# Kernel tuning notes

Hardware: AMD Instinct MI355X
Metric: run time of the kernel (lower is better)

The kernel has to match this reference:

```python
import jax, jax.numpy as jnp
import numpy as np

B, N, QD = 2, 4096, 512
HEADS, DIM_HEAD = 8, 64
INNER = HEADS * DIM_HEAD  # 512
SCALE = DIM_HEAD ** -0.5


def setup_inputs() -> dict:
    key = jax.random.key(0)
    ks = jax.random.split(key, 6)
    s = 0.02
    return {
        "x": jax.random.normal(ks[0], (B, N, QD), dtype=jnp.float32),
        "Wq": jax.random.normal(ks[1], (QD, INNER), dtype=jnp.float32) * s,
        "Wk": jax.random.normal(ks[2], (QD, INNER), dtype=jnp.float32) * s,
        "Wv": jax.random.normal(ks[3], (QD, INNER), dtype=jnp.float32) * s,
        "Wo": jax.random.normal(ks[4], (INNER, QD), dtype=jnp.float32) * s,
        "bo": jnp.zeros((QD,), dtype=jnp.float32),
    }


def reference(x, Wq, Wk, Wv, Wo, bo):
    # self-attention: context = x; mask = None; attention_sf = False
    q = x @ Wq  # [B, N, INNER]
    k = x @ Wk
    v = x @ Wv
    # split heads: [B, H, N, D]
    def split(t):
        return t.reshape(B, N, HEADS, DIM_HEAD).transpose(0, 2, 1, 3)
    q, k, v = split(q), split(k), split(v)
    # fp32 QK^T (ATTN_PRECISION='fp32' path)
    sim = jnp.einsum('bhid,bhjd->bhij', q.astype(jnp.float32), k.astype(jnp.float32)) * SCALE
    attn = jax.nn.softmax(sim, axis=-1)
    out = jnp.einsum('bhij,bhjd->bhid', attn, v)  # [B, H, N, D]
    out = out.transpose(0, 2, 1, 3).reshape(B, N, INNER)
    return out @ Wo + bo  # Dropout(p=0) is identity
```

## Files before the change

kernel.cpp:

```cpp
#include <hip/hip_runtime.h>
#include <hip/hip_bf16.h>


typedef __attribute__((ext_vector_type(8))) short short8;
typedef __attribute__((ext_vector_type(4))) float floatx4;

#define MFMA16(a, b, c) __builtin_amdgcn_mfma_f32_16x16x32_bf16((a), (b), (c), 0, 0, 0)

#if __has_builtin(__builtin_amdgcn_exp2f)
#define EXP2(x) __builtin_amdgcn_exp2f(x)
#else
#define EXP2(x) exp2f(x)
#endif

#define QSCALE 0.18033688011112042f

static __device__ __forceinline__ unsigned short f2b(float f) {
  unsigned int u = __float_as_uint(f);
  u += 0x7FFFu + ((u >> 16) & 1u);
  return (unsigned short)(u >> 16);
}

static __device__ __forceinline__ unsigned int pkb(float a, float b) {
  float2 t{a, b};
  __hip_bfloat162 h = __float22bfloat162_rn(t);
  union { __hip_bfloat162 h2; unsigned int u; } cv;
  cv.h2 = h;
  return cv.u;
}

static __device__ __forceinline__ void dma16(const unsigned short* g,
                                             unsigned short* l) {
  __builtin_amdgcn_global_load_lds(
      (const __attribute__((address_space(1))) unsigned int*)g,
      (__attribute__((address_space(3))) unsigned int*)l, 16, 0, 0);
}

__global__ __launch_bounds__(256) void prep_kernel(
    const float* __restrict__ Wq, const float* __restrict__ Wk,
    const float* __restrict__ Wv, const float* __restrict__ Wo,
    const float* __restrict__ x, unsigned short* __restrict__ wtq,
    unsigned short* __restrict__ wtk, unsigned short* __restrict__ wtv,
    unsigned short* __restrict__ wto, unsigned short* __restrict__ xb) {
  const int z = blockIdx.z;
  const int tid = threadIdx.x;
  if (z >= 4) {
    const int bid = (z - 4) * 256 + blockIdx.y * 16 + blockIdx.x;
    const int idx = (bid * 256 + tid) * 8;
    const float4 a = *(const float4*)(x + idx);
    const float4 b = *(const float4*)(x + idx + 4);
    unsigned int u[4] = {pkb(a.x, a.y), pkb(a.z, a.w), pkb(b.x, b.y),
                         pkb(b.z, b.w)};
    *(short8*)(xb + idx) = *(short8*)u;
    return;
  }
  const float* __restrict__ W = (z == 0) ? Wq : (z == 1) ? Wk : (z == 2) ? Wv : Wo;
  unsigned short* __restrict__ T = (z == 0) ? wtq : (z == 1) ? wtk : (z == 2) ? wtv : wto;
  const int k0 = blockIdx.x * 32, c0 = blockIdx.y * 32;
  __shared__ float Ts[32][33];
  const int r = tid >> 3, cc = (tid & 7) * 4;
  const float4 v = *(const float4*)(W + (k0 + r) * 512 + c0 + cc);
  Ts[r][cc] = v.x; Ts[r][cc + 1] = v.y; Ts[r][cc + 2] = v.z; Ts[r][cc + 3] = v.w;
  __syncthreads();
  const unsigned long long uu =
      (unsigned long long)pkb(Ts[cc][r], Ts[cc + 1][r]) |
      ((unsigned long long)pkb(Ts[cc + 2][r], Ts[cc + 3][r]) << 32);
  *(unsigned long long*)(T + (c0 + r) * 512 + k0 + cc) = uu;
}

__global__ __launch_bounds__(256) void qkv_fused_kernel(
    const float* __restrict__ x, const unsigned short* __restrict__ wtq,
    const unsigned short* __restrict__ wtk,
    const unsigned short* __restrict__ wtv, unsigned short* __restrict__ qo,
    unsigned short* __restrict__ ko, unsigned short* __restrict__ vo) {
  const int m0 = blockIdx.x * 128;
  const int c0 = blockIdx.y * 64;
  __shared__ __align__(16) unsigned short As[128 * 40];
  __shared__ __align__(16) unsigned short Bs[3][64 * 32];
  const int tid = threadIdx.x;
  const int lane = tid & 63, w = tid >> 6;
  const int i = lane & 15, q = lane >> 4;
  const int wy = w >> 1, wx = w & 1;
  const int arow = tid >> 1, ch = (tid & 1) * 16;
  const int br = w * 16 + (lane >> 2), bc8 = (lane & 3) * 8;
  const unsigned short* bg0 = wtq + (c0 + br) * 512 + bc8;
  const unsigned short* bg1 = wtk + (c0 + br) * 512 + bc8;
  const unsigned short* bg2 = wtv + (c0 + br) * 512 + bc8;
  unsigned short* bd0 = &Bs[0][(w * 16) * 32];
  unsigned short* bd1 = &Bs[1][(w * 16) * 32];
  unsigned short* bd2 = &Bs[2][(w * 16) * 32];
  floatx4 acc[3][4][2] = {};
  for (int k0 = 0; k0 < 512; k0 += 32) {
    dma16(bg0 + k0, bd0);
    dma16(bg1 + k0, bd1);
    dma16(bg2 + k0, bd2);
    {
      const float* src = x + (m0 + arow) * 512 + k0 + ch;
      unsigned int av[8];
#pragma unroll
      for (int j = 0; j < 8; ++j) av[j] = pkb(src[2 * j], src[2 * j + 1]);
      *(short8*)&As[arow * 40 + ch] = *(short8*)&av[0];
      *(short8*)&As[arow * 40 + ch + 8] = *(short8*)&av[4];
    }
    __syncthreads();
    short8 af[4];
#pragma unroll
    for (int t = 0; t < 4; ++t)
      af[t] = *(const short8*)&As[(wy * 64 + t * 16 + i) * 40 + q * 8];
#pragma unroll
    for (int z = 0; z < 3; ++z)
#pragma unroll
      for (int g = 0; g < 2; ++g) {
        const short8 bf =
            *(const short8*)&Bs[z][(wx * 32 + g * 16 + i) * 32 + q * 8];
#pragma unroll
        for (int t = 0; t < 4; ++t)
          acc[z][t][g] = MFMA16(af[t], bf, acc[z][t][g]);
      }
    __syncthreads();
  }
#pragma unroll
  for (int z = 0; z < 3; ++z)
#pragma unroll
    for (int t = 0; t < 4; ++t)
#pragma unroll
      for (int g = 0; g < 2; ++g) {
        const int col = c0 + wx * 32 + g * 16 + i;
        const int h = col >> 6, d = col & 63;
        const int row0 = m0 + wy * 64 + t * 16 + q * 4;
        const int b = row0 >> 12;
        const int n0 = row0 & 4095;
        if (z == 2) {
          unsigned int* dst =
              (unsigned int*)&vo[(((b * 8 + h) * 64 + d) << 12) + n0];
          dst[0] = pkb(acc[z][t][g][0], acc[z][t][g][1]);
          dst[1] = pkb(acc[z][t][g][2], acc[z][t][g][3]);
        } else {
          unsigned short* dst = (z == 0) ? qo : ko;
          const float sc = (z == 0) ? QSCALE : 1.0f;
#pragma unroll
          for (int r = 0; r < 4; ++r)
            dst[(((b * 8 + h) << 12) + (n0 + r)) * 64 + d] =
                f2b(acc[z][t][g][r] * sc);
        }
      }
}

__global__ __launch_bounds__(512, 4) void flash_kernel(
    const unsigned short* __restrict__ Q, const unsigned short* __restrict__ K,
    const unsigned short* __restrict__ Vt, unsigned short* __restrict__ O) {
  const int bh = blockIdx.x;
  const int m0 = blockIdx.y * 128;
  const int tid = threadIdx.x;
  const int lane = tid & 63, w = tid >> 6;
  const int i = lane & 15, q = lane >> 4;
  const int rt = w & 3;
  const int kg = w >> 2;
  const unsigned short* qp = Q + bh * (4096 * 64);
  const unsigned short* kp = K + bh * (4096 * 64);
  const unsigned short* vp = Vt + bh * (64 * 4096);

  __shared__ __align__(16) unsigned short SM[32768];
  unsigned short* Ks = SM + kg * 4096;
  unsigned short* Vs = SM + 8192 + kg * 4096;
  unsigned short* pw = SM + 16384 + w * 2048;

  const int srow = (tid & 255) >> 3;
  const int c0s = tid & 7;
  const int sw8 = (c0s ^ (srow & 7)) * 8;
  const unsigned short* kgp = kp + (kg * 2048 + srow) * 64 + c0s * 8;
  const unsigned short* vgp = vp + srow * 4096 + kg * 2048 + c0s * 8;

  short8 qf[2][2];
#pragma unroll
  for (int t = 0; t < 2; ++t)
#pragma unroll
    for (int kc = 0; kc < 2; ++kc)
      qf[t][kc] = *(const short8*)(qp + (m0 + rt * 32 + t * 16 + i) * 64 +
                                   kc * 32 + q * 8);

  floatx4 accO[2][4] = {};
  floatx4 accL[2] = {};
  short8 ones;
  {
    const short ov = (i == 0) ? (short)0x3F80 : (short)0;
#pragma unroll
    for (int j = 0; j < 8; ++j) ones[j] = ov;
  }
  const floatx4 zf = {0.f, 0.f, 0.f, 0.f};
  const int sl = i & 7;

  *(short8*)&Ks[srow * 64 + sw8] = *(const short8*)(kgp);
  *(short8*)&Ks[(srow + 32) * 64 + sw8] = *(const short8*)(kgp + 32 * 64);
  *(short8*)&Vs[srow * 64 + sw8] = *(const short8*)(vgp);
  *(short8*)&Vs[(srow + 32) * 64 + sw8] = *(const short8*)(vgp + 32 * 4096);
  __syncthreads();

  for (int jt = 0; jt < 32; ++jt) {
    short8 kn0, kn1, vn0, vn1;
    if (jt < 31) {
      kn0 = *(const short8*)(kgp + (jt + 1) * 4096);
      kn1 = *(const short8*)(kgp + (jt + 1) * 4096 + 32 * 64);
      vn0 = *(const short8*)(vgp + (jt + 1) * 64);
      vn1 = *(const short8*)(vgp + (jt + 1) * 64 + 32 * 4096);
    }
#pragma unroll
    for (int g = 0; g < 4; ++g) {
      const short8 kf0 = *(const short8*)(&Ks[(g * 16 + i) * 64 + (q ^ sl) * 8]);
      const short8 kf1 =
          *(const short8*)(&Ks[(g * 16 + i) * 64 + ((4 + q) ^ sl) * 8]);
#pragma unroll
      for (int t = 0; t < 2; ++t) {
        floatx4 s = MFMA16(kf0, qf[t][0], zf);
        s = MFMA16(kf1, qf[t][1], s);
        const float e0 = EXP2(s[0]), e1 = EXP2(s[1]);
        const float e2 = EXP2(s[2]), e3 = EXP2(s[3]);
        *(unsigned long long*)&pw[(t * 16 + i) * 64 +
                                  (((2 * g + (q >> 1)) ^ sl) * 8) +
                                  (q & 1) * 4] =
            (unsigned long long)pkb(e0, e1) |
            ((unsigned long long)pkb(e2, e3) << 32);
      }
    }
    short8 pf[2][2];
#pragma unroll
    for (int t = 0; t < 2; ++t) {
      pf[t][0] = *(const short8*)(pw + (t * 16 + i) * 64 + (q ^ sl) * 8);
      pf[t][1] = *(const short8*)(pw + (t * 16 + i) * 64 + ((4 + q) ^ sl) * 8);
      accL[t] = MFMA16(pf[t][0], ones, accL[t]);
      accL[t] = MFMA16(pf[t][1], ones, accL[t]);
    }
#pragma unroll
    for (int dg = 0; dg < 4; ++dg) {
      const short8 vf0 =
          *(const short8*)(&Vs[(dg * 16 + i) * 64 + (q ^ sl) * 8]);
      const short8 vf1 =
          *(const short8*)(&Vs[(dg * 16 + i) * 64 + ((4 + q) ^ sl) * 8]);
#pragma unroll
      for (int t = 0; t < 2; ++t) {
        accO[t][dg] = MFMA16(pf[t][0], vf0, accO[t][dg]);
        accO[t][dg] = MFMA16(pf[t][1], vf1, accO[t][dg]);
      }
    }
    __syncthreads();
    if (jt < 31) {
      *(short8*)&Ks[srow * 64 + sw8] = kn0;
      *(short8*)&Ks[(srow + 32) * 64 + sw8] = kn1;
      *(short8*)&Vs[srow * 64 + sw8] = vn0;
      *(short8*)&Vs[(srow + 32) * 64 + sw8] = vn1;
    }
    __syncthreads();
  }

  float* MB = (float*)SM;
  if (kg == 1) {
    float* dst = MB + (rt * 64 + lane) * 40;
#pragma unroll
    for (int t = 0; t < 2; ++t) {
#pragma unroll
      for (int dg = 0; dg < 4; ++dg)
#pragma unroll
        for (int r = 0; r < 4; ++r) dst[t * 16 + dg * 4 + r] = accO[t][dg][r];
#pragma unroll
      for (int r = 0; r < 4; ++r) dst[32 + t * 4 + r] = accL[t][r];
    }
  }
  __syncthreads();
  if (kg == 1) return;
  {
    const float* src = MB + (rt * 64 + lane) * 40;
#pragma unroll
    for (int t = 0; t < 2; ++t) {
#pragma unroll
      for (int dg = 0; dg < 4; ++dg)
#pragma unroll
        for (int r = 0; r < 4; ++r) accO[t][dg][r] += src[t * 16 + dg * 4 + r];
#pragma unroll
      for (int r = 0; r < 4; ++r) accL[t][r] += src[32 + t * 4 + r];
    }
  }

  const int b = bh >> 3, h = bh & 7;
#pragma unroll
  for (int t = 0; t < 2; ++t) {
    float inv[4];
#pragma unroll
    for (int r = 0; r < 4; ++r) {
      const float l = __shfl(accL[t][r], lane & 48, 64);
      inv[r] = 1.0f / l;
    }
#pragma unroll
    for (int dg = 0; dg < 4; ++dg)
#pragma unroll
      for (int r = 0; r < 4; ++r) {
        const int n = m0 + rt * 32 + t * 16 + q * 4 + r;
        const int col = h * 64 + dg * 16 + i;
        O[((b << 12) + n) * 512 + col] = f2b(accO[t][dg][r] * inv[r]);
      }
  }
}

__global__ __launch_bounds__(256) void out_proj_kernel(
    const unsigned short* __restrict__ A, const unsigned short* __restrict__ wto,
    const float* __restrict__ bo, float* __restrict__ out) {
  const int m0 = blockIdx.x * 64, c0 = blockIdx.y * 64;
  __shared__ __align__(16) unsigned short As[64 * 32];
  __shared__ __align__(16) unsigned short Bs[64 * 32];
  const int tid = threadIdx.x;
  const int lane = tid & 63, w = tid >> 6;
  const int i = lane & 15, q = lane >> 4;
  const int wy = w >> 1, wx = w & 1;
  const int sr = lane >> 2, sc8 = (lane & 3) * 8;
  const unsigned short* ag = A + (m0 + w * 16 + sr) * 512 + sc8;
  const unsigned short* bg = wto + (c0 + w * 16 + sr) * 512 + sc8;
  unsigned short* adst = &As[(w * 16) * 32];
  unsigned short* bdst = &Bs[(w * 16) * 32];
  floatx4 acc[2][2] = {};
  for (int k0 = 0; k0 < 512; k0 += 32) {
    dma16(ag + k0, adst);
    dma16(bg + k0, bdst);
    __syncthreads();
    short8 af[2], bfr[2];
#pragma unroll
    for (int t = 0; t < 2; ++t)
      af[t] = *(const short8*)&As[(wy * 32 + t * 16 + i) * 32 + q * 8];
#pragma unroll
    for (int g = 0; g < 2; ++g)
      bfr[g] = *(const short8*)&Bs[(wx * 32 + g * 16 + i) * 32 + q * 8];
#pragma unroll
    for (int t = 0; t < 2; ++t)
#pragma unroll
      for (int g = 0; g < 2; ++g) acc[t][g] = MFMA16(af[t], bfr[g], acc[t][g]);
    __syncthreads();
  }
#pragma unroll
  for (int t = 0; t < 2; ++t)
#pragma unroll
    for (int g = 0; g < 2; ++g) {
      const int col = c0 + wx * 32 + g * 16 + i;
      const float bias = bo[col];
#pragma unroll
      for (int r = 0; r < 4; ++r) {
        const int row = m0 + wy * 32 + t * 16 + q * 4 + r;
        out[row * 512 + col] = acc[t][g][r] + bias;
      }
    }
}

extern "C" void kernel_launch(void* const* d_in, const int* in_sizes, int n_in,
                              void* d_out, int out_size, void* d_ws,
                              size_t ws_size, hipStream_t stream) {
  const float* x = (const float*)d_in[0];
  const float* Wq = (const float*)d_in[1];
  const float* Wk = (const float*)d_in[2];
  const float* Wv = (const float*)d_in[3];
  const float* Wo = (const float*)d_in[4];
  const float* bo = (const float*)d_in[5];
  float* out = (float*)d_out;

  const size_t tsz = (size_t)16 * 4096 * 64;
  unsigned short* qws = (unsigned short*)d_ws;
  unsigned short* kws = qws + tsz;
  unsigned short* vws = kws + tsz;
  unsigned short* ows = vws + tsz;
  unsigned short* wtq = ows + tsz;
  unsigned short* wtk = wtq + 512 * 512;
  unsigned short* wtv = wtk + 512 * 512;
  unsigned short* wto = wtv + 512 * 512;
  unsigned short* xb = wto + 512 * 512;

  prep_kernel<<<dim3(16, 16, 12), 256, 0, stream>>>(Wq, Wk, Wv, Wo, x, wtq,
                                                    wtk, wtv, wto, xb);
  qkv_fused_kernel<<<dim3(64, 8), 256, 0, stream>>>(x, wtq, wtk, wtv, qws, kws,
                                                    vws);
  flash_kernel<<<dim3(16, 32), 512, 0, stream>>>(qws, kws, vws, ows);
  out_proj_kernel<<<dim3(128, 8), 256, 0, stream>>>(ows, wto, bo, out);
}
```

Measured before the change: 194.3 us.

## Double-buffer QKV and out-proj GEMMs with swizzled LDS and bf16 x input

Both projection GEMMs now double-buffer their LDS tiles, prefetching the next 64-wide K slice by DMA while MFMAs run on the current one. The K step grows from 32 to 64 and the LDS layout gains an XOR swizzle to avoid bank conflicts. The QKV kernel now reads the bf16 x already produced by the prep kernel instead of converting fp32 x in the loop. Its tile shrinks to 128x32 per block with a 1x4 warp layout, doubling the grid to get more blocks in flight. The cost is more LDS per block and less register reuse per wave in the QKV kernel.

```diff
diff --git a/kernel.cpp b/kernel.cpp
--- a/kernel.cpp
+++ b/kernel.cpp
@@ -69,65 +69,75 @@
 }
 
 __global__ __launch_bounds__(256) void qkv_fused_kernel(
-    const float* __restrict__ x, const unsigned short* __restrict__ wtq,
+    const unsigned short* __restrict__ xb, const unsigned short* __restrict__ wtq,
     const unsigned short* __restrict__ wtk,
     const unsigned short* __restrict__ wtv, unsigned short* __restrict__ qo,
     unsigned short* __restrict__ ko, unsigned short* __restrict__ vo) {
   const int m0 = blockIdx.x * 128;
-  const int c0 = blockIdx.y * 64;
-  __shared__ __align__(16) unsigned short As[128 * 40];
-  __shared__ __align__(16) unsigned short Bs[3][64 * 32];
+  const int c0 = blockIdx.y * 32;
+  __shared__ __align__(16) unsigned short As[2][128 * 64];
+  __shared__ __align__(16) unsigned short Bs[2][3][32 * 64];
   const int tid = threadIdx.x;
   const int lane = tid & 63, w = tid >> 6;
   const int i = lane & 15, q = lane >> 4;
-  const int wy = w >> 1, wx = w & 1;
-  const int arow = tid >> 1, ch = (tid & 1) * 16;
-  const int br = w * 16 + (lane >> 2), bc8 = (lane & 3) * 8;
-  const unsigned short* bg0 = wtq + (c0 + br) * 512 + bc8;
-  const unsigned short* bg1 = wtk + (c0 + br) * 512 + bc8;
-  const unsigned short* bg2 = wtv + (c0 + br) * 512 + bc8;
-  unsigned short* bd0 = &Bs[0][(w * 16) * 32];
-  unsigned short* bd1 = &Bs[1][(w * 16) * 32];
-  unsigned short* bd2 = &Bs[2][(w * 16) * 32];
-  floatx4 acc[3][4][2] = {};
-  for (int k0 = 0; k0 < 512; k0 += 32) {
-    dma16(bg0 + k0, bd0);
-    dma16(bg1 + k0, bd1);
-    dma16(bg2 + k0, bd2);
-    {
-      const float* src = x + (m0 + arow) * 512 + k0 + ch;
-      unsigned int av[8];
-#pragma unroll
-      for (int j = 0; j < 8; ++j) av[j] = pkb(src[2 * j], src[2 * j + 1]);
-      *(short8*)&As[arow * 40 + ch] = *(short8*)&av[0];
-      *(short8*)&As[arow * 40 + ch + 8] = *(short8*)&av[4];
+  const int sl = i & 7;
+  const int dr = lane >> 3, dc = lane & 7;
+  const int sch = (dc ^ dr) * 8;
+  const unsigned short* ag = xb + (m0 + w * 32 + dr) * 512 + sch;
+  const unsigned short* bg[3];
+  bg[0] = wtq + (c0 + w * 8 + dr) * 512 + sch;
+  bg[1] = wtk + (c0 + w * 8 + dr) * 512 + sch;
+  bg[2] = wtv + (c0 + w * 8 + dr) * 512 + sch;
+
+  floatx4 acc[3][2][2] = {};
+
+#pragma unroll
+  for (int p = 0; p < 4; ++p) dma16(ag + p * 8 * 512, &As[0][(w * 32 + p * 8) * 64]);
+#pragma unroll
+  for (int z = 0; z < 3; ++z) dma16(bg[z], &Bs[0][z][(w * 8) * 64]);
+  __syncthreads();
+
+  int buf = 0;
+  for (int ks = 0; ks < 8; ++ks) {
+    if (ks < 7) {
+      const int k1 = (ks + 1) * 64;
+#pragma unroll
+      for (int p = 0; p < 4; ++p)
+        dma16(ag + p * 8 * 512 + k1, &As[buf ^ 1][(w * 32 + p * 8) * 64]);
+#pragma unroll
+      for (int z = 0; z < 3; ++z)
+        dma16(bg[z] + k1, &Bs[buf ^ 1][z][(w * 8) * 64]);
+    }
+#pragma unroll
+    for (int kc = 0; kc < 2; ++kc) {
+      short8 af[2];
+#pragma unroll
+      for (int t = 0; t < 2; ++t)
+        af[t] = *(const short8*)&As[buf][(w * 32 + t * 16 + i) * 64 +
+                                        (((kc * 4 + q) ^ sl) * 8)];
+#pragma unroll
+      for (int z = 0; z < 3; ++z)
+#pragma unroll
+        for (int g = 0; g < 2; ++g) {
+          const short8 bf = *(const short8*)&Bs[buf][z][(g * 16 + i) * 64 +
+                                                        (((kc * 4 + q) ^ sl) * 8)];
+#pragma unroll
+          for (int t = 0; t < 2; ++t)
+            acc[z][t][g] = MFMA16(af[t], bf, acc[z][t][g]);
+        }
     }
     __syncthreads();
-    short8 af[4];
-#pragma unroll
-    for (int t = 0; t < 4; ++t)
-      af[t] = *(const short8*)&As[(wy * 64 + t * 16 + i) * 40 + q * 8];
-#pragma unroll
-    for (int z = 0; z < 3; ++z)
+    buf ^= 1;
+  }
+#pragma unroll
+  for (int z = 0; z < 3; ++z)
+#pragma unroll
+    for (int t = 0; t < 2; ++t)
 #pragma unroll
       for (int g = 0; g < 2; ++g) {
-        const short8 bf =
-            *(const short8*)&Bs[z][(wx * 32 + g * 16 + i) * 32 + q * 8];
-#pragma unroll
-        for (int t = 0; t < 4; ++t)
-          acc[z][t][g] = MFMA16(af[t], bf, acc[z][t][g]);
-      }
-    __syncthreads();
-  }
-#pragma unroll
-  for (int z = 0; z < 3; ++z)
-#pragma unroll
-    for (int t = 0; t < 4; ++t)
-#pragma unroll
-      for (int g = 0; g < 2; ++g) {
-        const int col = c0 + wx * 32 + g * 16 + i;
+        const int col = c0 + g * 16 + i;
         const int h = col >> 6, d = col & 63;
-        const int row0 = m0 + wy * 64 + t * 16 + q * 4;
+        const int row0 = m0 + w * 32 + t * 16 + q * 4;
         const int b = row0 >> 12;
         const int n0 = row0 & 4095;
         if (z == 2) {
@@ -304,34 +314,54 @@
     const unsigned short* __restrict__ A, const unsigned short* __restrict__ wto,
     const float* __restrict__ bo, float* __restrict__ out) {
   const int m0 = blockIdx.x * 64, c0 = blockIdx.y * 64;
-  __shared__ __align__(16) unsigned short As[64 * 32];
-  __shared__ __align__(16) unsigned short Bs[64 * 32];
+  __shared__ __align__(16) unsigned short As[2][64 * 64];
+  __shared__ __align__(16) unsigned short Bs[2][64 * 64];
   const int tid = threadIdx.x;
   const int lane = tid & 63, w = tid >> 6;
   const int i = lane & 15, q = lane >> 4;
   const int wy = w >> 1, wx = w & 1;
-  const int sr = lane >> 2, sc8 = (lane & 3) * 8;
-  const unsigned short* ag = A + (m0 + w * 16 + sr) * 512 + sc8;
-  const unsigned short* bg = wto + (c0 + w * 16 + sr) * 512 + sc8;
-  unsigned short* adst = &As[(w * 16) * 32];
-  unsigned short* bdst = &Bs[(w * 16) * 32];
+  const int sl = i & 7;
+  const int dr = lane >> 3, dc = lane & 7;
+  const int sch = (dc ^ dr) * 8;
+  const unsigned short* ag = A + (m0 + w * 16 + dr) * 512 + sch;
+  const unsigned short* bg = wto + (c0 + w * 16 + dr) * 512 + sch;
+
   floatx4 acc[2][2] = {};
-  for (int k0 = 0; k0 < 512; k0 += 32) {
-    dma16(ag + k0, adst);
-    dma16(bg + k0, bdst);
+#pragma unroll
+  for (int p = 0; p < 2; ++p) {
+    dma16(ag + p * 8 * 512, &As[0][(w * 16 + p * 8) * 64]);
+    dma16(bg + p * 8 * 512, &Bs[0][(w * 16 + p * 8) * 64]);
+  }
+  __syncthreads();
+
+  int buf = 0;
+  for (int ks = 0; ks < 8; ++ks) {
+    if (ks < 7) {
+      const int k1 = (ks + 1) * 64;
+#pragma unroll
+      for (int p = 0; p < 2; ++p) {
+        dma16(ag + p * 8 * 512 + k1, &As[buf ^ 1][(w * 16 + p * 8) * 64]);
+        dma16(bg + p * 8 * 512 + k1, &Bs[buf ^ 1][(w * 16 + p * 8) * 64]);
+      }
+    }
+#pragma unroll
+    for (int kc = 0; kc < 2; ++kc) {
+      short8 af[2], bfr[2];
+#pragma unroll
+      for (int t = 0; t < 2; ++t)
+        af[t] = *(const short8*)&As[buf][(wy * 32 + t * 16 + i) * 64 +
+                                        (((kc * 4 + q) ^ sl) * 8)];
+#pragma unroll
+      for (int g = 0; g < 2; ++g)
+        bfr[g] = *(const short8*)&Bs[buf][(wx * 32 + g * 16 + i) * 64 +
+                                          (((kc * 4 + q) ^ sl) * 8)];
+#pragma unroll
+      for (int t = 0; t < 2; ++t)
+#pragma unroll
+        for (int g = 0; g < 2; ++g) acc[t][g] = MFMA16(af[t], bfr[g], acc[t][g]);
+    }
     __syncthreads();
-    short8 af[2], bfr[2];
-#pragma unroll
-    for (int t = 0; t < 2; ++t)
-      af[t] = *(const short8*)&As[(wy * 32 + t * 16 + i) * 32 + q * 8];
-#pragma unroll
-    for (int g = 0; g < 2; ++g)
-      bfr[g] = *(const short8*)&Bs[(wx * 32 + g * 16 + i) * 32 + q * 8];
-#pragma unroll
-    for (int t = 0; t < 2; ++t)
-#pragma unroll
-      for (int g = 0; g < 2; ++g) acc[t][g] = MFMA16(af[t], bfr[g], acc[t][g]);
-    __syncthreads();
+    buf ^= 1;
   }
 #pragma unroll
   for (int t = 0; t < 2; ++t)
@@ -371,8 +401,8 @@
 
   prep_kernel<<<dim3(16, 16, 12), 256, 0, stream>>>(Wq, Wk, Wv, Wo, x, wtq,
                                                     wtk, wtv, wto, xb);
-  qkv_fused_kernel<<<dim3(64, 8), 256, 0, stream>>>(x, wtq, wtk, wtv, qws, kws,
-                                                    vws);
+  qkv_fused_kernel<<<dim3(64, 16), 256, 0, stream>>>(xb, wtq, wtk, wtv, qws,
+                                                     kws, vws);
   flash_kernel<<<dim3(16, 32), 512, 0, stream>>>(qws, kws, vws, ows);
   out_proj_kernel<<<dim3(128, 8), 256, 0, stream>>>(ows, wto, bo, out);
 }
```

Result: no change. 192.7 us, median of 2 (-0.8%).
